# Kernel optimization log

Measured on AMD Instinct MI355X. Metric: run time of the kernel, lower is better.

Reference implementation:

```python
import jax, jax.numpy as jnp
import numpy as np

N, E, FIN, NH, FOUT = 50000, 800000, 128, 4, 16


def setup_inputs() -> dict:
    key = jax.random.key(0)
    ks = jax.random.split(key, 6)
    x = jax.random.normal(ks[0], (N, FIN), dtype=jnp.float32)
    edge_index = jax.random.randint(ks[1], (2, E), 0, N, dtype=jnp.int64)
    w_proj = jax.random.normal(ks[2], (NH * FOUT, FIN), dtype=jnp.float32) * 0.05
    a_src = jax.random.normal(ks[3], (NH, FOUT), dtype=jnp.float32) * 0.1
    a_trg = jax.random.normal(ks[4], (NH, FOUT), dtype=jnp.float32) * 0.1
    w_skip = jax.random.normal(ks[5], (NH * FOUT, FIN), dtype=jnp.float32) * 0.05
    return {"x": x, "edge_index": edge_index, "w_proj": w_proj,
            "a_src": a_src, "a_trg": a_trg, "w_skip": w_skip}


def reference(x, edge_index, w_proj, a_src, a_trg, w_skip):
    # Dropout is identity in eval mode.
    src, trg = edge_index[0], edge_index[1]
    # Project: [N, NH, FOUT]
    proj = (x @ w_proj.T).reshape(N, NH, FOUT)
    # Per-node attention logits: [N, NH]
    s_src = jnp.einsum('nhf,hf->nh', proj, a_src)
    s_trg = jnp.einsum('nhf,hf->nh', proj, a_trg)
    # Lift to edges and score: [E, NH]
    scores = jax.nn.leaky_relu(s_src[src] + s_trg[trg], negative_slope=0.2)
    # Global-max-shifted exp (matches original, which subtracts the global max)
    exp_scores = jnp.exp(scores - jnp.max(scores))
    # Segment-wise softmax denominator over target nodes
    denom = jax.ops.segment_sum(exp_scores, trg, num_segments=N)  # [N, NH]
    attn = exp_scores / (denom[trg] + 1e-16)                      # [E, NH]
    # Weighted aggregation of lifted source features: [N, NH, FOUT]
    weighted = proj[src] * attn[:, :, None]
    agg = jax.ops.segment_sum(weighted, trg, num_segments=N)
    # Skip projection (FOUT != FIN branch) and concat over heads
    out = agg + (x @ w_skip.T).reshape(N, NH, FOUT)
    out = out.reshape(N, NH * FOUT)
    return jax.nn.elu(out)
```

## Files before the change

### kernel.cpp

```cpp
#include <hip/hip_runtime.h>
#include <cstddef>

#define N_NODES 50000
#define N_EDGES 800000
#define FIN     128
#define NH      4
#define FOUT    16
#define COUT    64
#define STRIPS  (N_NODES / 16)
#define SCAN_BLOCKS ((N_NODES + 255) / 256)
#define NB      128
#define CHUNK   (N_EDGES / NB)
#define HW4     (N_NODES / 4)
#define HBYTES  (HW4 * 4)
#define NQ      4
#define BPQ     (NB / NQ)
#define PBLK    ((HW4 + 255) / 256)

typedef __bf16 bf16x8 __attribute__((ext_vector_type(8)));
typedef float  f32x4  __attribute__((ext_vector_type(4)));

__global__ __launch_bounds__(256) void k0_init(
    const float* __restrict__ wproj, const float* __restrict__ wskip,
    __bf16* __restrict__ wb)
{
    int gid = blockIdx.x * 256 + threadIdx.x;
    if (gid < (128 * FIN) / 4) {
        int row = gid >> 5;
        float4 v = (row < 64) ? reinterpret_cast<const float4*>(wproj)[gid]
                              : reinterpret_cast<const float4*>(wskip)[gid - 2048];
        __bf16* o = wb + (size_t)gid * 4;
        o[0] = (__bf16)v.x; o[1] = (__bf16)v.y;
        o[2] = (__bf16)v.z; o[3] = (__bf16)v.w;
    }
}

__global__ __launch_bounds__(256) void k1_mfma(
    const float* __restrict__ x, const __bf16* __restrict__ wb,
    const float* __restrict__ asrc, const float* __restrict__ atrg,
    __bf16* __restrict__ projb, float* __restrict__ ssrc, float* __restrict__ strg,
    float* __restrict__ outv)
{
    const int lane  = threadIdx.x & 63;
    const int wid   = blockIdx.x * 4 + (threadIdx.x >> 6);
    const int strip = wid >> 1;
    const int half  = wid & 1;
    if (strip >= STRIPS) return;
    const int r = lane & 15;
    const int g = lane >> 4;
    const int row0 = strip * 16;

    bf16x8 bfr[4][4];
    #pragma unroll
    for (int j = 0; j < 4; ++j) {
        const __bf16* wrow = wb + (size_t)(half * 64 + j * 16 + r) * FIN;
        #pragma unroll
        for (int kk = 0; kk < 4; ++kk)
            bfr[j][kk] = *reinterpret_cast<const bf16x8*>(wrow + kk * 32 + g * 8);
    }

    const float* xrow = x + (size_t)(row0 + r) * FIN + g * 8;
    bf16x8 afr[4];
    #pragma unroll
    for (int kk = 0; kk < 4; ++kk) {
        float4 u0 = *reinterpret_cast<const float4*>(xrow + kk * 32);
        float4 u1 = *reinterpret_cast<const float4*>(xrow + kk * 32 + 4);
        bf16x8 a;
        a[0] = (__bf16)u0.x; a[1] = (__bf16)u0.y;
        a[2] = (__bf16)u0.z; a[3] = (__bf16)u0.w;
        a[4] = (__bf16)u1.x; a[5] = (__bf16)u1.y;
        a[6] = (__bf16)u1.z; a[7] = (__bf16)u1.w;
        afr[kk] = a;
    }

    f32x4 acc[4] = {{0.f,0.f,0.f,0.f},{0.f,0.f,0.f,0.f},
                    {0.f,0.f,0.f,0.f},{0.f,0.f,0.f,0.f}};
    #pragma unroll
    for (int kk = 0; kk < 4; ++kk)
        #pragma unroll
        for (int j = 0; j < 4; ++j)
            acc[j] = __builtin_amdgcn_mfma_f32_16x16x32_bf16(
                         afr[kk], bfr[j][kk], acc[j], 0, 0, 0);

    if (!half) {
        #pragma unroll
        for (int j = 0; j < 4; ++j)
            #pragma unroll
            for (int q = 0; q < 4; ++q)
                projb[(size_t)(row0 + g * 4 + q) * COUT + j * 16 + r] =
                    (__bf16)acc[j][q];
        #pragma unroll
        for (int j = 0; j < 4; ++j) {
            const float as = asrc[j * 16 + r];
            const float at = atrg[j * 16 + r];
            #pragma unroll
            for (int q = 0; q < 4; ++q) {
                float ts = acc[j][q] * as;
                float tt = acc[j][q] * at;
                ts += __shfl_xor(ts, 1); ts += __shfl_xor(ts, 2);
                ts += __shfl_xor(ts, 4); ts += __shfl_xor(ts, 8);
                tt += __shfl_xor(tt, 1); tt += __shfl_xor(tt, 2);
                tt += __shfl_xor(tt, 4); tt += __shfl_xor(tt, 8);
                if (r == 0) {
                    int n = row0 + g * 4 + q;
                    ssrc[(size_t)n * NH + j] = ts;
                    strg[(size_t)n * NH + j] = tt;
                }
            }
        }
    } else {
        #pragma unroll
        for (int j = 0; j < 4; ++j)
            #pragma unroll
            for (int q = 0; q < 4; ++q)
                outv[(size_t)(row0 + g * 4 + q) * COUT + j * 16 + r] = acc[j][q];
    }
}

__global__ __launch_bounds__(1024) void k_hist(
    const int* __restrict__ ei, unsigned* __restrict__ histG)
{
    extern __shared__ unsigned h[];
    const int t = threadIdx.x;
    for (int i = t; i < HW4; i += 1024) h[i] = 0;
    __syncthreads();
    const int base = blockIdx.x * CHUNK;
    for (int i = t; i < CHUNK; i += 1024) {
        int tg = ei[N_EDGES + base + i];
        atomicAdd(&h[tg >> 2], 1u << ((tg & 3) * 8));
    }
    __syncthreads();
    unsigned* out = histG + (size_t)blockIdx.x * HW4;
    for (int i = t; i < HW4; i += 1024) out[i] = h[i];
}

__global__ __launch_bounds__(256) void k_colscanA(
    const unsigned* __restrict__ histG, unsigned* __restrict__ offG,
    unsigned* __restrict__ partial)
{
    int p = blockIdx.x * 256 + threadIdx.x;
    if (p >= HW4) return;
    int q = blockIdx.y;
    unsigned run = 0;
    #pragma unroll 4
    for (int b = q * BPQ; b < (q + 1) * BPQ; ++b) {
        unsigned v = histG[(size_t)b * HW4 + p];
        offG[(size_t)b * HW4 + p] = run;
        run += v;
    }
    partial[(size_t)q * HW4 + p] = run;
}

__global__ __launch_bounds__(256) void k_colscanB(
    const unsigned* __restrict__ partial, unsigned* __restrict__ baseQ,
    int* __restrict__ deg)
{
    int p = blockIdx.x * 256 + threadIdx.x;
    if (p >= HW4) return;
    unsigned s = 0;
    #pragma unroll
    for (int q = 0; q < NQ; ++q) {
        baseQ[(size_t)q * HW4 + p] = s;
        s += partial[(size_t)q * HW4 + p];
    }
    reinterpret_cast<int4*>(deg)[p] =
        make_int4((int)(s & 0xffu), (int)((s >> 8) & 0xffu),
                  (int)((s >> 16) & 0xffu), (int)(s >> 24));
}

__global__ __launch_bounds__(256) void scan_a(
    const int* __restrict__ deg, int* __restrict__ tmpExc, int* __restrict__ bsum)
{
    __shared__ int sm[256];
    int t = threadIdx.x;
    int i = blockIdx.x * 256 + t;
    int v = (i < N_NODES) ? deg[i] : 0;
    sm[t] = v; __syncthreads();
    #pragma unroll
    for (int off = 1; off < 256; off <<= 1) {
        int x = (t >= off) ? sm[t - off] : 0;
        __syncthreads();
        sm[t] += x;
        __syncthreads();
    }
    if (i < N_NODES) tmpExc[i] = sm[t] - v;
    if (t == 255) bsum[blockIdx.x] = sm[t];
}

__global__ __launch_bounds__(256) void scan_b(
    const int* __restrict__ bsum, int* __restrict__ bOff)
{
    __shared__ int sm[256];
    int t = threadIdx.x;
    int v = (t < SCAN_BLOCKS) ? bsum[t] : 0;
    sm[t] = v; __syncthreads();
    #pragma unroll
    for (int off = 1; off < 256; off <<= 1) {
        int x = (t >= off) ? sm[t - off] : 0;
        __syncthreads();
        sm[t] += x;
        __syncthreads();
    }
    if (t < SCAN_BLOCKS) bOff[t] = sm[t] - v;
}

__global__ __launch_bounds__(1024) void k_place(
    const int* __restrict__ ei, const unsigned* __restrict__ offG,
    const unsigned* __restrict__ baseQ,
    const int* __restrict__ tmpExc, const int* __restrict__ bOff,
    int* __restrict__ srcs)
{
    extern __shared__ unsigned h[];
    const int t = threadIdx.x;
    for (int i = t; i < HW4; i += 1024) h[i] = 0;
    __syncthreads();
    const int base = blockIdx.x * CHUNK;
    const unsigned* off = offG  + (size_t)blockIdx.x * HW4;
    const unsigned* bq  = baseQ + (size_t)(blockIdx.x / BPQ) * HW4;
    for (int i = t; i < CHUNK; i += 1024) {
        int s  = ei[base + i];
        int tg = ei[N_EDGES + base + i];
        int sh = (tg & 3) * 8;
        unsigned old = atomicAdd(&h[tg >> 2], 1u << sh);
        int local = (int)((old >> sh) & 0xffu);
        unsigned cw = off[tg >> 2] + bq[tg >> 2];
        int cross = (int)((cw >> sh) & 0xffu);
        int slot  = tmpExc[tg] + bOff[tg >> 8] + cross + local;
        srcs[slot] = s;
    }
}

__global__ __launch_bounds__(256) void k3_gather(
    const int* __restrict__ tmpExc, const int* __restrict__ bOff,
    const int* __restrict__ deg, const int* __restrict__ srcs,
    const float* __restrict__ ssrc, const float* __restrict__ strg,
    const __bf16* __restrict__ projb, float* __restrict__ outv)
{
    const int lane = threadIdx.x & 63;
    const int node = __builtin_amdgcn_readfirstlane(blockIdx.x * 4 + (threadIdx.x >> 6));
    if (node >= N_NODES) return;
    const int h = lane >> 4;
    const int begin = tmpExc[node] + bOff[node >> 8];
    const int dg    = deg[node];
    const float st  = strg[(size_t)node * NH + h];
    const float skip = outv[(size_t)node * COUT + lane];

    float acc = 0.f, dsum = 0.f;
    int i = 0;
    for (; i + 8 <= dg; i += 8) {
        int s[8]; float a[8], p[8];
        #pragma unroll
        for (int u = 0; u < 8; ++u) s[u] = srcs[begin + i + u];
        #pragma unroll
        for (int u = 0; u < 8; ++u) a[u] = ssrc[(size_t)s[u] * NH + h];
        #pragma unroll
        for (int u = 0; u < 8; ++u) p[u] = (float)projb[(size_t)s[u] * COUT + lane];
        #pragma unroll
        for (int u = 0; u < 8; ++u) {
            float z = a[u] + st;
            z = (z >= 0.f) ? z : 0.2f * z;
            float ez = __expf(z);
            dsum += ez;
            acc += ez * p[u];
        }
    }
    for (; i + 4 <= dg; i += 4) {
        int s[4]; float a[4], p[4];
        #pragma unroll
        for (int u = 0; u < 4; ++u) s[u] = srcs[begin + i + u];
        #pragma unroll
        for (int u = 0; u < 4; ++u) a[u] = ssrc[(size_t)s[u] * NH + h];
        #pragma unroll
        for (int u = 0; u < 4; ++u) p[u] = (float)projb[(size_t)s[u] * COUT + lane];
        #pragma unroll
        for (int u = 0; u < 4; ++u) {
            float z = a[u] + st;
            z = (z >= 0.f) ? z : 0.2f * z;
            float ez = __expf(z);
            dsum += ez;
            acc += ez * p[u];
        }
    }
    for (; i < dg; ++i) {
        int s = srcs[begin + i];
        float z = ssrc[(size_t)s * NH + h] + st;
        z = (z >= 0.f) ? z : 0.2f * z;
        float ez = __expf(z);
        float p  = (float)projb[(size_t)s * COUT + lane];
        dsum += ez;
        acc += ez * p;
    }
    float o = acc / (dsum + 1e-16f) + skip;
    o = (o > 0.f) ? o : expm1f(o);
    outv[(size_t)node * COUT + lane] = o;
}

extern "C" void kernel_launch(void* const* d_in, const int* in_sizes, int n_in,
                              void* d_out, int out_size, void* d_ws, size_t ws_size,
                              hipStream_t stream)
{
    const float* x     = (const float*)d_in[0];
    const int*   ei    = (const int*)  d_in[1];
    const float* wproj = (const float*)d_in[2];
    const float* asrc  = (const float*)d_in[3];
    const float* atrg  = (const float*)d_in[4];
    const float* wskip = (const float*)d_in[5];
    float* outv = (float*)d_out;

    __bf16* projb = (__bf16*)d_ws;
    float* base  = (float*)d_ws;
    float* ssrc  = base + (size_t)N_NODES * COUT;
    float* strg  = ssrc + (size_t)N_NODES * NH;
    int* deg     = (int*)(strg + (size_t)N_NODES * NH);
    int* tmpExc  = deg    + N_NODES;
    int* bsum    = tmpExc + N_NODES;
    int* bOff    = bsum   + 256;
    int* srcs    = bOff   + 256;
    unsigned* histG   = (unsigned*)(srcs + N_EDGES);
    unsigned* offG    = histG + (size_t)NB * HW4;
    unsigned* partial = offG  + (size_t)NB * HW4;
    unsigned* baseQ   = partial + (size_t)NQ * HW4;
    __bf16* wb   = (__bf16*)(baseQ + (size_t)NQ * HW4);

    k0_init<<<16, 256, 0, stream>>>(wproj, wskip, wb);

    int k1_blocks = (STRIPS * 2 + 3) / 4;
    k1_mfma<<<k1_blocks, 256, 0, stream>>>(x, wb, asrc, atrg,
                                           projb, ssrc, strg, outv);

    k_hist<<<NB, 1024, HBYTES, stream>>>(ei, histG);

    k_colscanA<<<dim3(PBLK, NQ), 256, 0, stream>>>(histG, offG, partial);
    k_colscanB<<<PBLK, 256, 0, stream>>>(partial, baseQ, deg);

    scan_a<<<SCAN_BLOCKS, 256, 0, stream>>>(deg, tmpExc, bsum);
    scan_b<<<1, 256, 0, stream>>>(bsum, bOff);

    k_place<<<NB, 1024, HBYTES, stream>>>(ei, offG, baseQ, tmpExc, bOff, srcs);

    int k3_blocks = (N_NODES + 3) / 4;
    k3_gather<<<k3_blocks, 256, 0, stream>>>(tmpExc, bOff, deg, srcs,
                                             ssrc, strg, projb, outv);
}
```

Before: 108.7 us.

## Record per-edge rank in histogram pass and fuse column scan with degree scan

```diff
diff --git a/kernel.cpp b/kernel.cpp
--- a/kernel.cpp
+++ b/kernel.cpp
@@ -16,6 +16,8 @@
 #define NQ      4
 #define BPQ     (NB / NQ)
 #define PBLK    ((HW4 + 255) / 256)
+#define E4      (N_EDGES / 4)
+#define E4B     ((E4 + 255) / 256)
 
 typedef __bf16 bf16x8 __attribute__((ext_vector_type(8)));
 typedef float  f32x4  __attribute__((ext_vector_type(4)));
@@ -118,7 +120,8 @@
 }
 
 __global__ __launch_bounds__(1024) void k_hist(
-    const int* __restrict__ ei, unsigned* __restrict__ histG)
+    const int* __restrict__ ei, unsigned* __restrict__ histG,
+    unsigned char* __restrict__ rank)
 {
     extern __shared__ unsigned h[];
     const int t = threadIdx.x;
@@ -127,7 +130,9 @@
     const int base = blockIdx.x * CHUNK;
     for (int i = t; i < CHUNK; i += 1024) {
         int tg = ei[N_EDGES + base + i];
-        atomicAdd(&h[tg >> 2], 1u << ((tg & 3) * 8));
+        int sh = (tg & 3) * 8;
+        unsigned old = atomicAdd(&h[tg >> 2], 1u << sh);
+        rank[base + i] = (unsigned char)((old >> sh) & 0xffu);
     }
     __syncthreads();
     unsigned* out = histG + (size_t)blockIdx.x * HW4;
@@ -151,31 +156,33 @@
     partial[(size_t)q * HW4 + p] = run;
 }
 
-__global__ __launch_bounds__(256) void k_colscanB(
+__global__ __launch_bounds__(256) void k_scanfuse(
     const unsigned* __restrict__ partial, unsigned* __restrict__ baseQ,
-    int* __restrict__ deg)
-{
-    int p = blockIdx.x * 256 + threadIdx.x;
-    if (p >= HW4) return;
-    unsigned s = 0;
-    #pragma unroll
-    for (int q = 0; q < NQ; ++q) {
-        baseQ[(size_t)q * HW4 + p] = s;
-        s += partial[(size_t)q * HW4 + p];
-    }
-    reinterpret_cast<int4*>(deg)[p] =
-        make_int4((int)(s & 0xffu), (int)((s >> 8) & 0xffu),
-                  (int)((s >> 16) & 0xffu), (int)(s >> 24));
-}
-
-__global__ __launch_bounds__(256) void scan_a(
-    const int* __restrict__ deg, int* __restrict__ tmpExc, int* __restrict__ bsum)
+    int* __restrict__ deg, int* __restrict__ tmpExc, int* __restrict__ bsum)
 {
     __shared__ int sm[256];
-    int t = threadIdx.x;
-    int i = blockIdx.x * 256 + t;
-    int v = (i < N_NODES) ? deg[i] : 0;
-    sm[t] = v; __syncthreads();
+    const int t = threadIdx.x;
+    if (t < 64) {
+        int p = blockIdx.x * 64 + t;
+        if (p < HW4) {
+            unsigned s = 0;
+            #pragma unroll
+            for (int q = 0; q < NQ; ++q) {
+                baseQ[(size_t)q * HW4 + p] = s;
+                s += partial[(size_t)q * HW4 + p];
+            }
+            int4 d4 = make_int4((int)(s & 0xffu), (int)((s >> 8) & 0xffu),
+                                (int)((s >> 16) & 0xffu), (int)(s >> 24));
+            reinterpret_cast<int4*>(deg)[p] = d4;
+            sm[4 * t + 0] = d4.x; sm[4 * t + 1] = d4.y;
+            sm[4 * t + 2] = d4.z; sm[4 * t + 3] = d4.w;
+        } else {
+            sm[4 * t + 0] = 0; sm[4 * t + 1] = 0;
+            sm[4 * t + 2] = 0; sm[4 * t + 3] = 0;
+        }
+    }
+    __syncthreads();
+    int v = sm[t];
     #pragma unroll
     for (int off = 1; off < 256; off <<= 1) {
         int x = (t >= off) ? sm[t - off] : 0;
@@ -183,6 +190,7 @@
         sm[t] += x;
         __syncthreads();
     }
+    int i = blockIdx.x * 256 + t;
     if (i < N_NODES) tmpExc[i] = sm[t] - v;
     if (t == 255) bsum[blockIdx.x] = sm[t];
 }
@@ -204,29 +212,31 @@
     if (t < SCAN_BLOCKS) bOff[t] = sm[t] - v;
 }
 
-__global__ __launch_bounds__(1024) void k_place(
-    const int* __restrict__ ei, const unsigned* __restrict__ offG,
-    const unsigned* __restrict__ baseQ,
+__global__ __launch_bounds__(256) void k_scatter(
+    const int* __restrict__ ei, const unsigned char* __restrict__ rank,
+    const unsigned* __restrict__ offG, const unsigned* __restrict__ baseQ,
     const int* __restrict__ tmpExc, const int* __restrict__ bOff,
     int* __restrict__ srcs)
 {
-    extern __shared__ unsigned h[];
-    const int t = threadIdx.x;
-    for (int i = t; i < HW4; i += 1024) h[i] = 0;
-    __syncthreads();
-    const int base = blockIdx.x * CHUNK;
-    const unsigned* off = offG  + (size_t)blockIdx.x * HW4;
-    const unsigned* bq  = baseQ + (size_t)(blockIdx.x / BPQ) * HW4;
-    for (int i = t; i < CHUNK; i += 1024) {
-        int s  = ei[base + i];
-        int tg = ei[N_EDGES + base + i];
+    int e4 = blockIdx.x * 256 + threadIdx.x;
+    if (e4 >= E4) return;
+    int4 s4 = reinterpret_cast<const int4*>(ei)[e4];
+    int4 t4 = reinterpret_cast<const int4*>(ei + N_EDGES)[e4];
+    uchar4 r4 = reinterpret_cast<const uchar4*>(rank)[e4];
+    const int e0 = e4 * 4;
+    int ss[4] = {s4.x, s4.y, s4.z, s4.w};
+    int tt[4] = {t4.x, t4.y, t4.z, t4.w};
+    int rr[4] = {r4.x, r4.y, r4.z, r4.w};
+    #pragma unroll
+    for (int u = 0; u < 4; ++u) {
+        int tg = tt[u];
+        int b  = (e0 + u) / CHUNK;
         int sh = (tg & 3) * 8;
-        unsigned old = atomicAdd(&h[tg >> 2], 1u << sh);
-        int local = (int)((old >> sh) & 0xffu);
-        unsigned cw = off[tg >> 2] + bq[tg >> 2];
+        unsigned cw = offG[(size_t)b * HW4 + (tg >> 2)]
+                    + baseQ[(size_t)(b / BPQ) * HW4 + (tg >> 2)];
         int cross = (int)((cw >> sh) & 0xffu);
-        int slot  = tmpExc[tg] + bOff[tg >> 8] + cross + local;
-        srcs[slot] = s;
+        int slot  = tmpExc[tg] + bOff[tg >> 8] + cross + rr[u];
+        srcs[slot] = ss[u];
     }
 }
 
@@ -320,7 +330,8 @@
     unsigned* offG    = histG + (size_t)NB * HW4;
     unsigned* partial = offG  + (size_t)NB * HW4;
     unsigned* baseQ   = partial + (size_t)NQ * HW4;
-    __bf16* wb   = (__bf16*)(baseQ + (size_t)NQ * HW4);
+    unsigned char* rank = (unsigned char*)(baseQ + (size_t)NQ * HW4);
+    __bf16* wb   = (__bf16*)(rank + N_EDGES);
 
     k0_init<<<16, 256, 0, stream>>>(wproj, wskip, wb);
 
@@ -328,15 +339,16 @@
     k1_mfma<<<k1_blocks, 256, 0, stream>>>(x, wb, asrc, atrg,
                                            projb, ssrc, strg, outv);
 
-    k_hist<<<NB, 1024, HBYTES, stream>>>(ei, histG);
+    k_hist<<<NB, 1024, HBYTES, stream>>>(ei, histG, rank);
 
     k_colscanA<<<dim3(PBLK, NQ), 256, 0, stream>>>(histG, offG, partial);
-    k_colscanB<<<PBLK, 256, 0, stream>>>(partial, baseQ, deg);
-
-    scan_a<<<SCAN_BLOCKS, 256, 0, stream>>>(deg, tmpExc, bsum);
+
+    k_scanfuse<<<SCAN_BLOCKS, 256, 0, stream>>>(partial, baseQ, deg,
+                                                tmpExc, bsum);
     scan_b<<<1, 256, 0, stream>>>(bsum, bOff);
 
-    k_place<<<NB, 1024, HBYTES, stream>>>(ei, offG, baseQ, tmpExc, bOff, srcs);
+    k_scatter<<<E4B, 256, 0, stream>>>(ei, rank, offG, baseQ,
+                                       tmpExc, bOff, srcs);
 
     int k3_blocks = (N_NODES + 3) / 4;
     k3_gather<<<k3_blocks, 256, 0, stream>>>(tmpExc, bOff, deg, srcs,
```

Result: faster. 99.29 us (-8.7%).
